# Kernel optimization log

Hardware: AMD Instinct MI355X
Metric: run time of the kernel (lower is better)

The kernel has to match this reference:

```python
import jax, jax.numpy as jnp
import numpy as np

THETA = 10000.0
NUM_HEADS = 16
MAX_SEQ_LEN = 2048

def _rope_tables(d_k, max_seq_len, theta=THETA):
    dims = jnp.arange(0, d_k, 2, dtype=jnp.float32)
    freqs = 1.0 / theta ** (dims / d_k)
    t = jnp.arange(max_seq_len, dtype=jnp.float32)
    angles = jnp.outer(t, freqs)  # (max_seq_len, d_k//2)
    return jnp.cos(angles), jnp.sin(angles)

def _apply_rope(x, token_positions, cos_tab, sin_tab):
    # x: (..., seq_len, d_k)
    cos = jnp.repeat(cos_tab[token_positions], 2, axis=-1)  # (seq_len, d_k)
    sin = jnp.repeat(sin_tab[token_positions], 2, axis=-1)
    # interleaved rotate-half: (-x1, x0, -x3, x2, ...)
    xp = x.reshape(*x.shape[:-1], -1, 2)
    x_neg = jnp.stack([-xp[..., 1], xp[..., 0]], axis=-1).reshape(x.shape)
    return x * cos + x_neg * sin

def setup_inputs() -> dict:
    key = jax.random.key(0)
    ks = jax.random.split(key, 5)
    B, S, D = 4, 2048, 1024
    scale = 1.0 / np.sqrt(D)
    return {
        "x": jax.random.normal(ks[0], (B, S, D), dtype=jnp.float32),
        "q_proj": jax.random.normal(ks[1], (D, D), dtype=jnp.float32) * scale,
        "k_proj": jax.random.normal(ks[2], (D, D), dtype=jnp.float32) * scale,
        "v_proj": jax.random.normal(ks[3], (D, D), dtype=jnp.float32) * scale,
        "o_proj": jax.random.normal(ks[4], (D, D), dtype=jnp.float32) * scale,
        "token_positions": jnp.arange(S, dtype=jnp.int64),
    }

def reference(x, q_proj, k_proj, v_proj, o_proj, token_positions):
    B, S, D = x.shape
    H = NUM_HEADS
    d_k = D // H
    cos_tab, sin_tab = _rope_tables(d_k, MAX_SEQ_LEN)

    q = (x @ q_proj).reshape(B, S, H, d_k).transpose(0, 2, 1, 3)  # (B,H,S,d_k)
    k = (x @ k_proj).reshape(B, S, H, d_k).transpose(0, 2, 1, 3)
    v = (x @ v_proj).reshape(B, S, H, d_k).transpose(0, 2, 1, 3)

    q = _apply_rope(q, token_positions, cos_tab, sin_tab)
    k = _apply_rope(k, token_positions, cos_tab, sin_tab)

    scores = jnp.einsum('bhqd,bhkd->bhqk', q, k) / jnp.sqrt(jnp.float32(d_k))
    causal = jnp.tril(jnp.ones((S, S), dtype=bool))
    scores = jnp.where(causal, scores, -jnp.inf)
    attn = jax.nn.softmax(scores, axis=-1)
    out = jnp.einsum('bhqk,bhkd->bhqd', attn, v)  # (B,H,S,d_k)
    out = out.transpose(0, 2, 1, 3).reshape(B, S, D)
    return out @ o_proj
```

## Files before the change

### kernel.cpp

```cpp
#include <hip/hip_runtime.h>
#include <hip/hip_bf16.h>
#include <stdint.h>


typedef __attribute__((ext_vector_type(8))) short short8;
typedef __attribute__((ext_vector_type(4))) float floatx4;
typedef __attribute__((ext_vector_type(16))) float floatx16;

#define MFMA16(a,b,c) __builtin_amdgcn_mfma_f32_16x16x32_bf16((a),(b),(c),0,0,0)
#define MFMA32(a,b,c) __builtin_amdgcn_mfma_f32_32x32x16_bf16((a),(b),(c),0,0,0)

__device__ __forceinline__ uint32_t fbits(float f){ uint32_t u; __builtin_memcpy(&u,&f,4); return u; }
__device__ __forceinline__ unsigned short f2bf(float f) {
    uint32_t u = fbits(f);
    return (unsigned short)((u + 0x7fffu + ((u>>16)&1u)) >> 16);
}
__device__ __forceinline__ float bf2f(unsigned short s){ uint32_t u = (uint32_t)s<<16; float f; __builtin_memcpy(&f,&u,4); return f; }
__device__ __forceinline__ uint32_t pkbf(float lo, float hi) {
    return __builtin_amdgcn_perm(fbits(hi)+0x8000u, fbits(lo)+0x8000u, 0x07060302u);
}

__device__ __forceinline__ void load_lds16(const unsigned short* g, unsigned short* l) {
    __builtin_amdgcn_global_load_lds(
        (const __attribute__((address_space(1))) void*)g,
        (__attribute__((address_space(3))) void*)l, 16, 0, 0);
}

__device__ __forceinline__ bool sniff_f32(const unsigned short* xr) {
    int lane = threadIdx.x & 63;
    int bad = 0;
#pragma unroll
    for (int i = 0; i < 16; i++) {
        float v = bf2f(xr[lane * 16 + i]);
        if (!(__builtin_fabsf(v) < 1e10f)) bad = 1;
    }
    return __ballot(bad != 0) != 0ull;
}

__global__ __launch_bounds__(256) void prep_k(
    const void* __restrict__ x,
    const void* __restrict__ wq, const void* __restrict__ wk,
    const void* __restrict__ wv, const void* __restrict__ wo,
    unsigned short* __restrict__ WT, unsigned short* __restrict__ WoT,
    float2* __restrict__ tab, unsigned short* __restrict__ xb) {
    int blk = blockIdx.x, t = threadIdx.x;
    bool f32 = sniff_f32((const unsigned short*)x);
    if (blk < 4096) {
        __shared__ unsigned short tile[32][33];
        int mat = blk >> 10, r = blk & 1023;
        const void* src = (mat == 0) ? wq : (mat == 1) ? wk : (mat == 2) ? wv : wo;
        unsigned short* dst = (mat < 3) ? (WT + (size_t)mat * 1048576) : WoT;
        int bx = (r & 31) * 32, by = (r >> 5) * 32;
        int tx = t & 31, ty = t >> 5;
#pragma unroll
        for (int j = 0; j < 32; j += 8) {
            size_t idx = (size_t)(by + ty + j) * 1024 + bx + tx;
            float v = f32 ? ((const float*)src)[idx] : bf2f(((const unsigned short*)src)[idx]);
            tile[ty + j][tx] = f2bf(v);
        }
        __syncthreads();
#pragma unroll
        for (int j = 0; j < 32; j += 8)
            dst[(size_t)(bx + ty + j) * 1024 + by + tx] = tile[tx][ty + j];
    } else if (blk < 4352) {
        int i = (blk - 4096) * 256 + t;
        int pos = i >> 5, j = i & 31;
        float freq = exp2f(-(float)(2 * j) * (1.0f / 64.0f) * 13.287712379549449f);
        float a = (float)pos * freq;
        tab[i] = make_float2(cosf(a), sinf(a));
    } else {
        size_t base = (size_t)(blk - 4352) * 2048 + (size_t)t * 8;
        if (f32) {
            const float4* s4 = (const float4*)((const float*)x + base);
            float4 a = s4[0], b = s4[1];
            uint4 o;
            o.x = pkbf(a.x, a.y); o.y = pkbf(a.z, a.w);
            o.z = pkbf(b.x, b.y); o.w = pkbf(b.z, b.w);
            *(uint4*)(xb + base) = o;
        } else {
            *(uint4*)(xb + base) = *(const uint4*)((const unsigned short*)x + base);
        }
    }
}

template <int MODE>
__global__ __launch_bounds__(256) void gemm_bt(
    const unsigned short* __restrict__ A,
    const unsigned short* __restrict__ Bt,
    void* __restrict__ C0,
    unsigned short* __restrict__ C1,
    unsigned short* __restrict__ C2,
    const float2* __restrict__ tab,
    const unsigned short* __restrict__ xsniff) {
    const int K = 1024;
    __shared__ __align__(16) unsigned short Al[128 * 32];
    __shared__ __align__(16) unsigned short Bl[128 * 32];

    int m0 = blockIdx.y * 128;
    int n0 = blockIdx.x * 128;
    int t = threadIdx.x;
    int lane = t & 63, w = t >> 6;
    int quad = lane >> 4, l15 = lane & 15;
    int wm = (w >> 1) * 64, wn = (w & 1) * 64;

    floatx4 acc[4][4];
#pragma unroll
    for (int i = 0; i < 4; i++)
#pragma unroll
        for (int j = 0; j < 4; j++) acc[i][j] = (floatx4){0.f, 0.f, 0.f, 0.f};

    for (int k0 = 0; k0 < K; k0 += 32) {
#pragma unroll
        for (int c = 0; c < 2; c++) {
            load_lds16(A + (size_t)(m0 + w * 32 + c * 16 + (lane >> 2)) * K + k0 + (lane & 3) * 8,
                       &Al[(w * 32 + c * 16) * 32]);
        }
#pragma unroll
        for (int c = 0; c < 2; c++) {
            load_lds16(Bt + (size_t)(n0 + w * 32 + c * 16 + (lane >> 2)) * K + k0 + (lane & 3) * 8,
                       &Bl[(w * 32 + c * 16) * 32]);
        }
        asm volatile("s_waitcnt vmcnt(0)" ::: "memory");
        __syncthreads();

        short8 af[4], bfr[4];
#pragma unroll
        for (int i = 0; i < 4; i++)
            af[i] = *(const short8*)&Al[(wm + i * 16 + l15) * 32 + quad * 8];
#pragma unroll
        for (int j = 0; j < 4; j++)
            bfr[j] = *(const short8*)&Bl[(wn + j * 16 + l15) * 32 + quad * 8];
#pragma unroll
        for (int i = 0; i < 4; i++)
#pragma unroll
            for (int j = 0; j < 4; j++) acc[i][j] = MFMA16(af[i], bfr[j], acc[i][j]);
        __syncthreads();
    }

    bool out_f32 = (MODE == 0) ? sniff_f32(xsniff) : false;
#pragma unroll
    for (int i = 0; i < 4; i++) {
#pragma unroll
        for (int j = 0; j < 4; j++) {
            int col = n0 + wn + j * 16 + l15;
            int row0 = m0 + wm + i * 16 + quad * 4;
            if (MODE == 0) {
#pragma unroll
                for (int r = 0; r < 4; r++) {
                    size_t idx = (size_t)(row0 + r) * 1024 + col;
                    if (out_f32) ((float*)C0)[idx] = acc[i][j][r];
                    else ((unsigned short*)C0)[idx] = f2bf(acc[i][j][r]);
                }
            } else {
                int which = col >> 10, nn = col & 1023;
                int b = row0 >> 11, s0 = row0 & 2047;
                if (which == 2) {
                    int hh = nn >> 6, d = nn & 63;
                    uint32_t lo = pkbf(acc[i][j][0], acc[i][j][1]);
                    uint32_t hi = pkbf(acc[i][j][2], acc[i][j][3]);
                    *(uint64_t*)(C2 + ((size_t)((b * 16 + hh) * 64 + d)) * 2048 + s0) =
                        (uint64_t)lo | ((uint64_t)hi << 32);
                } else {
                    int d = nn & 63;
                    unsigned short* dst = (which == 0) ? (unsigned short*)C0 : C1;
                    float sc = (which == 0) ? 0.18033688011112042f : 1.0f;
#pragma unroll
                    for (int r = 0; r < 4; r++) {
                        int s = s0 + r;
                        float v = acc[i][j][r];
                        float pv = __shfl_xor(v, 1);
                        float2 cs = tab[(s << 5) + (d >> 1)];
                        float o = (d & 1) ? (v * cs.x + pv * cs.y) : (v * cs.x - pv * cs.y);
                        dst[((size_t)(b * 2048 + s)) * 1024 + nn] = f2bf(o * sc);
                    }
                }
            }
        }
    }
}

__global__ __launch_bounds__(256, 2) void flash_k(
    const unsigned short* __restrict__ Qb,
    const unsigned short* __restrict__ Kb,
    const unsigned short* __restrict__ Vt,
    unsigned short* __restrict__ A2) {
    __shared__ __align__(16) unsigned short Kl[2][64 * 64];
    __shared__ __align__(16) unsigned short Vl[2][64 * 64];

    int bh = blockIdx.x;
    int y = blockIdx.y;
    int qt = (y < 4) ? (7 - y) : (y - 4);
    int b = bh >> 4, h = bh & 15;
    int t = threadIdx.x, lane = t & 63, w = t >> 6;
    int l31 = lane & 31, half = lane >> 5;
    size_t base = ((size_t)b * 2048) * 1024 + h * 64;
    int q0w = qt * 256 + w * 64;

    short8 Qf[2][4];
#pragma unroll
    for (int nb = 0; nb < 2; nb++)
#pragma unroll
        for (int ks = 0; ks < 4; ks++)
            Qf[nb][ks] = *(const short8*)(Qb + base + (size_t)(q0w + nb * 32 + l31) * 1024 +
                                          ks * 16 + half * 8);

    floatx16 O[2][2];
#pragma unroll
    for (int i = 0; i < 2; i++)
#pragma unroll
        for (int j = 0; j < 2; j++) O[i][j] = (floatx16)0.0f;
    float lsum[2] = {0.f, 0.f};

    int nk = 4 * (qt + 1);

    int srow = t >> 2;
    const unsigned short* kg = Kb + base + (size_t)srow * 1024 + (t & 3) * 16;
    const unsigned short* vg = Vt + ((size_t)(bh * 64 + srow)) * 2048 + (t & 3) * 16;
    int sw0 = srow * 64 + ((((t & 3) * 2 + 0) ^ (srow & 7)) * 8);
    int sw1 = srow * 64 + ((((t & 3) * 2 + 1) ^ (srow & 7)) * 8);

    short8 rk0 = *(const short8*)(kg);
    short8 rk1 = *(const short8*)(kg + 8);
    short8 rv0 = *(const short8*)(vg);
    short8 rv1 = *(const short8*)(vg + 8);

    for (int kt = 0; kt < nk; kt++) {
        int k0 = kt * 64, bf = kt & 1;
        *(short8*)&Kl[bf][sw0] = rk0;
        *(short8*)&Kl[bf][sw1] = rk1;
        *(short8*)&Vl[bf][sw0] = rv0;
        *(short8*)&Vl[bf][sw1] = rv1;
        __syncthreads();
        if (kt + 1 < nk) {
            size_t ko = (size_t)(kt + 1) * 64;
            rk0 = *(const short8*)(kg + ko * 1024);
            rk1 = *(const short8*)(kg + ko * 1024 + 8);
            rv0 = *(const short8*)(vg + ko);
            rv1 = *(const short8*)(vg + ko + 8);
        }
#pragma unroll
        for (int mb = 0; mb < 2; mb++) {
            if (k0 + mb * 32 >= q0w + 64) continue;
            short8 Ka[4];
#pragma unroll
            for (int ks = 0; ks < 4; ks++)
                Ka[ks] = *(const short8*)&Kl[bf][(mb * 32 + l31) * 64 +
                                                 (((ks * 2 + half) ^ (l31 & 7)) * 8)];
            floatx16 Sc[2];
#pragma unroll
            for (int nb = 0; nb < 2; nb++) Sc[nb] = (floatx16)0.0f;
#pragma unroll
            for (int nb = 0; nb < 2; nb++)
#pragma unroll
                for (int ks = 0; ks < 4; ks++)
                    Sc[nb] = MFMA32(Ka[ks], Qf[nb][ks], Sc[nb]);

            bool domask = (k0 + mb * 32 + 31 > q0w);
            uint32_t pkm[2][8];
#pragma unroll
            for (int nb = 0; nb < 2; nb++) {
                float p[16];
#pragma unroll
                for (int e = 0; e < 16; e++) {
                    float v = exp2f(Sc[nb][e]);
                    if (domask) {
                        int kv = k0 + mb * 32 + (e & 3) + ((e >> 2) << 3) + half * 4;
                        int qq = q0w + nb * 32 + l31;
                        v = (kv > qq) ? 0.f : v;
                    }
                    p[e] = v;
                }
                float t0 = (p[0] + p[1]) + (p[2] + p[3]);
                float t1 = (p[4] + p[5]) + (p[6] + p[7]);
                float t2 = (p[8] + p[9]) + (p[10] + p[11]);
                float t3 = (p[12] + p[13]) + (p[14] + p[15]);
                lsum[nb] += (t0 + t1) + (t2 + t3);
#pragma unroll
                for (int jj = 0; jj < 8; jj++)
                    pkm[nb][jj] = pkbf(p[2 * jj], p[2 * jj + 1]);
            }

            short8 Va[2][2];
#pragma unroll
            for (int db = 0; db < 2; db++)
#pragma unroll
                for (int ks2 = 0; ks2 < 2; ks2++)
                    Va[db][ks2] = *(const short8*)&Vl[bf][(db * 32 + l31) * 64 +
                                                         ((((mb * 2 + ks2) * 2 + half) ^ (l31 & 7)) * 8)];
#pragma unroll
            for (int ks2 = 0; ks2 < 2; ks2++) {
#pragma unroll
                for (int nb = 0; nb < 2; nb++) {
                    uint32_t p0 = pkm[nb][4 * ks2 + 0];
                    uint32_t p1 = pkm[nb][4 * ks2 + 1];
                    uint32_t p2 = pkm[nb][4 * ks2 + 2];
                    uint32_t p3 = pkm[nb][4 * ks2 + 3];
                    uint32_t u = half ? p0 : p2;
                    uint32_t v2 = half ? p1 : p3;
                    uint32_t ya = (uint32_t)__shfl_xor((int)u, 32);
                    uint32_t yb = (uint32_t)__shfl_xor((int)v2, 32);
                    union { short8 s; uint32_t q[4]; } bb;
                    bb.q[0] = half ? ya : p0;
                    bb.q[1] = half ? yb : p1;
                    bb.q[2] = half ? p2 : ya;
                    bb.q[3] = half ? p3 : yb;
#pragma unroll
                    for (int db = 0; db < 2; db++)
                        O[db][nb] = MFMA32(Va[db][ks2], bb.s, O[db][nb]);
                }
            }
        }
    }

    float inv[2];
#pragma unroll
    for (int nb = 0; nb < 2; nb++) {
        float tot = lsum[nb] + __shfl_xor(lsum[nb], 32);
        inv[nb] = 1.0f / tot;
    }
#pragma unroll
    for (int db = 0; db < 2; db++) {
#pragma unroll
        for (int nb = 0; nb < 2; nb++) {
            int scol = q0w + nb * 32 + l31;
            unsigned short* op = A2 + base + (size_t)scol * 1024;
#pragma unroll
            for (int g = 0; g < 4; g++) {
                int d0 = db * 32 + half * 4 + g * 8;
                float v0 = O[db][nb][g * 4 + 0] * inv[nb];
                float v1 = O[db][nb][g * 4 + 1] * inv[nb];
                float v2 = O[db][nb][g * 4 + 2] * inv[nb];
                float v3 = O[db][nb][g * 4 + 3] * inv[nb];
                uint32_t lo = pkbf(v0, v1), hi = pkbf(v2, v3);
                *(uint64_t*)(op + d0) = (uint64_t)lo | ((uint64_t)hi << 32);
            }
        }
    }
}

extern "C" void kernel_launch(void* const* d_in, const int* in_sizes, int n_in,
                              void* d_out, int out_size, void* d_ws, size_t ws_size,
                              hipStream_t stream) {
    const void* x  = d_in[0];
    const void* wq = d_in[1];
    const void* wk = d_in[2];
    const void* wv = d_in[3];
    const void* wo = d_in[4];

    char* ws = (char*)d_ws;
    unsigned short* WT  = (unsigned short*)(ws);
    unsigned short* WoT = (unsigned short*)(ws + 6291456);
    float2*         tab = (float2*)(ws + 8388608);
    unsigned short* xb  = (unsigned short*)(ws + 8913920);
    unsigned short* Qb  = (unsigned short*)(ws + 8913920 + 16777216ull);
    unsigned short* Kb  = (unsigned short*)(ws + 8913920 + 2ull * 16777216);
    unsigned short* Vt  = (unsigned short*)(ws + 8913920 + 3ull * 16777216);
    unsigned short* A2  = xb;

    prep_k<<<8448, 256, 0, stream>>>(x, wq, wk, wv, wo, WT, WoT, tab, xb);

    gemm_bt<1><<<dim3(24, 64), 256, 0, stream>>>(xb, WT, Qb, Kb, Vt, tab,
                                                 (const unsigned short*)x);
    flash_k<<<dim3(64, 8), 256, 0, stream>>>(Qb, Kb, Vt, A2);
    gemm_bt<0><<<dim3(8, 64), 256, 0, stream>>>(A2, WoT, d_out, nullptr, nullptr, tab,
                                                (const unsigned short*)x);
}
```

Measured before the change: 300.7 us.

## Double-buffer LDS tiles in projection GEMM to overlap loads with MFMA

The bf16 GEMM used for the projections now keeps two LDS buffers for the A and B tiles. It issues the global-to-LDS loads for the next K slice before running the MFMAs on the current slice, which removes one barrier per step and hides global memory latency behind compute. In exchange it doubles the GEMM's LDS use, which may lower occupancy. It also keeps a full vmcnt(0) wait before each barrier.

```diff
diff --git a/kernel.cpp b/kernel.cpp
--- a/kernel.cpp
+++ b/kernel.cpp
@@ -93,8 +93,8 @@
     const float2* __restrict__ tab,
     const unsigned short* __restrict__ xsniff) {
     const int K = 1024;
-    __shared__ __align__(16) unsigned short Al[128 * 32];
-    __shared__ __align__(16) unsigned short Bl[128 * 32];
+    __shared__ __align__(16) unsigned short Al[2][128 * 32];
+    __shared__ __align__(16) unsigned short Bl[2][128 * 32];
 
     int m0 = blockIdx.y * 128;
     int n0 = blockIdx.x * 128;
@@ -109,31 +109,71 @@
 #pragma unroll
         for (int j = 0; j < 4; j++) acc[i][j] = (floatx4){0.f, 0.f, 0.f, 0.f};
 
-    for (int k0 = 0; k0 < K; k0 += 32) {
+    const unsigned short* ag[2];
+    const unsigned short* bg[2];
+    int lofs[2];
+#pragma unroll
+    for (int c = 0; c < 2; c++) {
+        int row = w * 32 + c * 16 + (lane >> 2);
+        ag[c] = A + (size_t)(m0 + row) * K + (lane & 3) * 8;
+        bg[c] = Bt + (size_t)(n0 + row) * K + (lane & 3) * 8;
+        lofs[c] = (w * 32 + c * 16) * 32;
+    }
+
+#pragma unroll
+    for (int c = 0; c < 2; c++) {
+        load_lds16(ag[c], &Al[0][lofs[c]]);
+        load_lds16(bg[c], &Bl[0][lofs[c]]);
+        ag[c] += 32; bg[c] += 32;
+    }
+    asm volatile("s_waitcnt vmcnt(0)" ::: "memory");
+    __syncthreads();
+
+    for (int kk = 0; kk < 16; kk++) {
 #pragma unroll
         for (int c = 0; c < 2; c++) {
-            load_lds16(A + (size_t)(m0 + w * 32 + c * 16 + (lane >> 2)) * K + k0 + (lane & 3) * 8,
-                       &Al[(w * 32 + c * 16) * 32]);
-        }
-#pragma unroll
-        for (int c = 0; c < 2; c++) {
-            load_lds16(Bt + (size_t)(n0 + w * 32 + c * 16 + (lane >> 2)) * K + k0 + (lane & 3) * 8,
-                       &Bl[(w * 32 + c * 16) * 32]);
+            load_lds16(ag[c], &Al[1][lofs[c]]);
+            load_lds16(bg[c], &Bl[1][lofs[c]]);
+            ag[c] += 32; bg[c] += 32;
+        }
+        {
+            short8 af[4], bfr[4];
+#pragma unroll
+            for (int i = 0; i < 4; i++)
+                af[i] = *(const short8*)&Al[0][(wm + i * 16 + l15) * 32 + quad * 8];
+#pragma unroll
+            for (int j = 0; j < 4; j++)
+                bfr[j] = *(const short8*)&Bl[0][(wn + j * 16 + l15) * 32 + quad * 8];
+#pragma unroll
+            for (int i = 0; i < 4; i++)
+#pragma unroll
+                for (int j = 0; j < 4; j++) acc[i][j] = MFMA16(af[i], bfr[j], acc[i][j]);
         }
         asm volatile("s_waitcnt vmcnt(0)" ::: "memory");
         __syncthreads();
 
-        short8 af[4], bfr[4];
-#pragma unroll
-        for (int i = 0; i < 4; i++)
-            af[i] = *(const short8*)&Al[(wm + i * 16 + l15) * 32 + quad * 8];
-#pragma unroll
-        for (int j = 0; j < 4; j++)
-            bfr[j] = *(const short8*)&Bl[(wn + j * 16 + l15) * 32 + quad * 8];
-#pragma unroll
-        for (int i = 0; i < 4; i++)
-#pragma unroll
-            for (int j = 0; j < 4; j++) acc[i][j] = MFMA16(af[i], bfr[j], acc[i][j]);
+        if (kk < 15) {
+#pragma unroll
+            for (int c = 0; c < 2; c++) {
+                load_lds16(ag[c], &Al[0][lofs[c]]);
+                load_lds16(bg[c], &Bl[0][lofs[c]]);
+                ag[c] += 32; bg[c] += 32;
+            }
+        }
+        {
+            short8 af[4], bfr[4];
+#pragma unroll
+            for (int i = 0; i < 4; i++)
+                af[i] = *(const short8*)&Al[1][(wm + i * 16 + l15) * 32 + quad * 8];
+#pragma unroll
+            for (int j = 0; j < 4; j++)
+                bfr[j] = *(const short8*)&Bl[1][(wn + j * 16 + l15) * 32 + quad * 8];
+#pragma unroll
+            for (int i = 0; i < 4; i++)
+#pragma unroll
+                for (int j = 0; j < 4; j++) acc[i][j] = MFMA16(af[i], bfr[j], acc[i][j]);
+        }
+        asm volatile("s_waitcnt vmcnt(0)" ::: "memory");
         __syncthreads();
     }
 
```

Measured after the change: 293.7 us. -2.3%, faster.
